# Kernel optimization log

Hardware: AMD Instinct MI355X
Metric: run time of the kernel (lower is better)

## Reference

```python
import jax, jax.numpy as jnp
import numpy as np

B, H, W, A, C = 8, 13, 13, 5, 20
ANCHORS = [[1.3221, 1.73145], [3.19275, 4.00944], [5.05587, 8.09892],
           [9.47112, 4.84053], [11.2364, 10.0071]]
L_COORD, OBJ_SCALE, NOOBJ_SCALE = 3.0, 5.0, 1.0
POS_FRAC_THRESH = 0.98


def gen_yolo_box():
    # anchor[..., 0:2] = (x_col, y_row) grid offsets, anchor[..., 2:4] = anchor (w, h)
    ys, xs = jnp.meshgrid(jnp.arange(H, dtype=jnp.float32),
                          jnp.arange(W, dtype=jnp.float32), indexing='ij')
    grid = jnp.broadcast_to(jnp.stack([xs, ys], -1)[:, :, None, :], (H, W, A, 2))
    wh = jnp.broadcast_to(jnp.asarray(ANCHORS, jnp.float32)[None, None], (H, W, A, 2))
    return jnp.concatenate([grid, wh], -1)  # [H, W, A, 4]


def decode(delta, anc, fs0, fs1):
    # delta: [..., 4] raw offsets; anc: [..., 4]; returns [x1, y1, w, h]
    w = jnp.exp(delta[..., 2]) * anc[..., 2] / fs0
    h = jnp.exp(delta[..., 3]) * anc[..., 3] / fs1
    x = (delta[..., 0] + anc[..., 0]) / fs0 - w * 0.5
    y = (delta[..., 1] + anc[..., 1]) / fs1 - h * 0.5
    return jnp.stack([x, y, w, h], -1)


def pairwise_iou(b1, b2):
    # b1: [N,4], b2: [M,4] in [x1,y1,w,h]; returns [N, M]
    b1x1, b1y1 = b1[:, 0:1], b1[:, 1:2]
    b1x2, b1y2 = b1x1 + b1[:, 2:3], b1y1 + b1[:, 3:4]
    b2x1, b2y1, b2x2, b2y2 = b2[:, 0], b2[:, 1], b2[:, 0] + b2[:, 2], b2[:, 1] + b2[:, 3]
    dx = jnp.clip(jnp.minimum(b1x2, b2x2[None, :]) - jnp.maximum(b1x1, b2x1[None, :]), 0)
    dy = jnp.clip(jnp.minimum(b1y2, b2y2[None, :]) - jnp.maximum(b1y1, b2y1[None, :]), 0)
    inter = dx * dy
    a1 = (b1x2 - b1x1) * (b1y2 - b1y1)          # [N,1]
    a2 = (b2x2 - b2x1) * (b2y2 - b2y1)          # [M]
    return inter / (a1 + a2[None, :] - inter)


def elem_iou(b1, b2):
    # elementwise IoU over [..., 4] boxes ([x1,y1,w,h])
    b1x2, b1y2 = b1[..., 0] + b1[..., 2], b1[..., 1] + b1[..., 3]
    b2x2, b2y2 = b2[..., 0] + b2[..., 2], b2[..., 1] + b2[..., 3]
    dx = jnp.clip(jnp.minimum(b1x2, b2x2) - jnp.maximum(b1[..., 0], b2[..., 0]), 0)
    dy = jnp.clip(jnp.minimum(b1y2, b2y2) - jnp.maximum(b1[..., 1], b2[..., 1]), 0)
    inter = dx * dy
    a1 = b1[..., 2] * b1[..., 3]
    a2 = b2[..., 2] * b2[..., 3]
    return inter / (a1 + a2 - inter)


def setup_inputs() -> dict:
    key = jax.random.key(0)
    ks = jax.random.split(key, 6)
    pred_cls = jax.random.normal(ks[0], (B, H, W, A, C), jnp.float32)
    pred_conf = jax.random.uniform(ks[1], (B, H, W, A, 1), jnp.float32)
    pred_bboxes = jax.random.normal(ks[2], (B, H, W, A, 4), jnp.float32)
    label_cls = jax.random.normal(ks[3], (B, H, W, A, C), jnp.float32)
    u = jax.random.uniform(ks[4], (B, H, W, A, 1), jnp.float32)
    label_conf = (u > POS_FRAC_THRESH).astype(jnp.float32)  # sparse positives
    label_bboxes = jax.random.uniform(ks[5], (B, H, W, A, 4), jnp.float32)
    return {"pred_cls": pred_cls, "pred_conf": pred_conf, "pred_bboxes": pred_bboxes,
            "label_cls": label_cls, "label_conf": label_conf, "label_bboxes": label_bboxes}


def reference(pred_cls, pred_conf, pred_bboxes, label_cls, label_conf, label_bboxes):
    dt = pred_bboxes.dtype
    fs0, fs1 = float(H), float(W)
    pos = label_conf[..., 0] > 0                 # [B,H,W,A]
    posf = pos.astype(dt)
    anc = gen_yolo_box()[None]                   # [1,H,W,A,4]

    gt_box = decode(label_bboxes, anc, fs0, fs1)   # [B,H,W,A,4]
    pred_box = decode(pred_bboxes, anc, fs0, fs1)  # [B,H,W,A,4]

    # "diagonal" IoU: each positive gt paired with the pred box at the same cell
    diag_iou = elem_iou(gt_box, pred_box)          # [B,H,W,A]
    p_conf = pred_conf[..., 0]
    loss_pos_conf = jnp.sum(posf * (p_conf - jax.lax.stop_gradient(diag_iou)) ** 2) \
        * OBJ_SCALE / B

    # dense masked pairwise IoU (gt rows masked to 0 where not positive)
    N = B * H * W * A
    iou_mat = pairwise_iou(gt_box.reshape(N, 4), pred_box.reshape(N, 4))  # [N,N]
    pos_flat = pos.reshape(N)
    iou_mat = jnp.where(pos_flat[:, None], iou_mat, jnp.zeros((), dt))
    best = jnp.max(iou_mat, axis=0)                       # per pred box
    best = jnp.where(pos_flat, jnp.ones((), dt), best)    # ious_[pos] = 1
    negf = (best < 0.6).astype(dt)
    loss_neg_conf = jnp.sum(negf * (p_conf.reshape(N) - label_conf.reshape(N)) ** 2) \
        * NOOBJ_SCALE / B

    # classification CE (sum) over positives
    logp = jax.nn.log_softmax(pred_cls, axis=-1)
    lbl = jnp.argmax(label_cls, axis=-1)
    nll = -jnp.take_along_axis(logp, lbl[..., None], axis=-1)[..., 0]
    loss_cls = jnp.sum(posf * nll) / B

    # coordinate losses over positives
    dxy = pred_bboxes[..., :2] - label_bboxes[..., :2]
    loss_x = jnp.sum(posf * dxy[..., 0] ** 2) * L_COORD / B
    loss_y = jnp.sum(posf * dxy[..., 1] ** 2) * L_COORD / B

    def huber(d):  # SmoothL1, beta=1
        ad = jnp.abs(d)
        return jnp.where(ad < 1.0, 0.5 * d * d, ad - 0.5)

    dwh = pred_bboxes[..., 2:4] - label_bboxes[..., 2:4]
    loss_w = jnp.sum(posf * huber(dwh[..., 0])) * L_COORD / B
    loss_h = jnp.sum(posf * huber(dwh[..., 1])) * L_COORD / B

    return loss_x + loss_y + loss_w + loss_h + loss_cls + loss_neg_conf + loss_pos_conf
```

## Files before the change

### kernel.cpp

```cpp
#include <hip/hip_runtime.h>

#define NB 8
#define HH 13
#define WW 13
#define AA 5
#define CC 20
#define NTOT (NB * HH * WW * AA)
#define L_COORD 3.0f
#define OBJ_SCALE 5.0f
#define INV_B (1.0f / 8.0f)
#define FS 13.0f
#define BLOCK 256
#define GRID ((NTOT + BLOCK - 1) / BLOCK)
#define CAP 4064
#define NCHUNK ((NTOT + CAP - 1) / CAP)
#define MAXITER 16

__device__ __constant__ float c_anc[AA][2] = {
    {1.3221f, 1.73145f}, {3.19275f, 4.00944f}, {5.05587f, 8.09892f},
    {9.47112f, 4.84053f}, {11.2364f, 10.0071f}};

__device__ __forceinline__ float block_reduce_sum(float v, float* sbuf) {
    for (int o = 32; o > 0; o >>= 1) v += __shfl_down(v, o);
    if ((threadIdx.x & 63) == 0) sbuf[threadIdx.x >> 6] = v;
    __syncthreads();
    float s = 0.f;
    if (threadIdx.x == 0) {
        for (int i = 0; i < (BLOCK >> 6); i++) s += sbuf[i];
    }
    return s;
}

__global__ void __launch_bounds__(BLOCK) yolo_fused_kernel(
    const float* __restrict__ pred_cls,
    const float* __restrict__ pred_conf,
    const float4* __restrict__ pred_bboxes,
    const float* __restrict__ label_cls,
    const float* __restrict__ label_conf,
    const float4* __restrict__ label_bboxes,
    float* __restrict__ out) {
    __shared__ float4 sbox[CAP];
    __shared__ int s_cnt;
    __shared__ float sred[BLOCK >> 6];

    const int tid = threadIdx.x;
    const int n   = blockIdx.x * BLOCK + tid;

    float local = 0.f;
    bool  neg   = false;
    float px1 = 0.f, py1 = 0.f, px2 = 0.f, py2 = 0.f, parea = 1.f, diffsq = 0.f;

    if (n < NTOT) {
        int a = n % AA;
        int w = (n / AA) % WW;
        int h = (n / (AA * WW)) % HH;
        float ancw = c_anc[a][0], anch = c_anc[a][1];

        float4 pb  = pred_bboxes[n];
        float  lcf = label_conf[n];
        float  pc  = pred_conf[n];

        float pw = expf(pb.z) * ancw * (1.f / FS);
        float ph = expf(pb.w) * anch * (1.f / FS);
        px1 = (pb.x + (float)w) * (1.f / FS) - pw * 0.5f;
        py1 = (pb.y + (float)h) * (1.f / FS) - ph * 0.5f;
        px2 = px1 + pw;
        py2 = py1 + ph;
        parea = pw * ph;

        if (lcf > 0.f) {
            float4 tb = label_bboxes[n];
            float gw = expf(tb.z) * ancw * (1.f / FS);
            float gh = expf(tb.w) * anch * (1.f / FS);
            float gx = (tb.x + (float)w) * (1.f / FS) - gw * 0.5f;
            float gy = (tb.y + (float)h) * (1.f / FS) - gh * 0.5f;
            float gx2 = gx + gw, gy2 = gy + gh;

            float dx = fminf(gx2, px2) - fmaxf(gx, px1); dx = fmaxf(dx, 0.f);
            float dy = fminf(gy2, py2) - fmaxf(gy, py1); dy = fmaxf(dy, 0.f);
            float inter = dx * dy;
            float iou = inter / (gw * gh + parea - inter);

            float dconf = pc - iou;
            local += OBJ_SCALE * dconf * dconf;

            const float4* lc4 = reinterpret_cast<const float4*>(label_cls) + (long)n * 5;
            const float4* pc4 = reinterpret_cast<const float4*>(pred_cls) + (long)n * 5;
            float lrow[CC], prow[CC];
            #pragma unroll
            for (int q = 0; q < 5; q++) {
                float4 v = lc4[q];
                lrow[4 * q + 0] = v.x; lrow[4 * q + 1] = v.y;
                lrow[4 * q + 2] = v.z; lrow[4 * q + 3] = v.w;
                float4 u = pc4[q];
                prow[4 * q + 0] = u.x; prow[4 * q + 1] = u.y;
                prow[4 * q + 2] = u.z; prow[4 * q + 3] = u.w;
            }
            int lbl = 0;
            float bl = lrow[0];
            #pragma unroll
            for (int i = 1; i < CC; i++) {
                if (lrow[i] > bl) { bl = lrow[i]; lbl = i; }
            }
            float mx = prow[0];
            #pragma unroll
            for (int i = 1; i < CC; i++) mx = fmaxf(mx, prow[i]);
            float s = 0.f;
            #pragma unroll
            for (int i = 0; i < CC; i++) s += expf(prow[i] - mx);
            local += mx + logf(s) - prow[lbl];

            float dxc = pb.x - tb.x, dyc = pb.y - tb.y;
            local += L_COORD * (dxc * dxc + dyc * dyc);
            float dwc = pb.z - tb.z, dhc = pb.w - tb.w;
            float adw = fabsf(dwc), adh = fabsf(dhc);
            float hw  = adw < 1.f ? 0.5f * dwc * dwc : adw - 0.5f;
            float hh2 = adh < 1.f ? 0.5f * dhc * dhc : adh - 0.5f;
            local += L_COORD * (hw + hh2);
        } else {
            neg = true;
            float d = pc - lcf;
            diffsq = d * d;
        }
    }

    float best = 0.f;
    for (int chunk = 0; chunk < NCHUNK; ++chunk) {
        const int base = chunk * CAP;
        const int rem  = min(CAP, NTOT - base);

        float cv[MAXITER];
        #pragma unroll
        for (int k = 0; k < MAXITER; k++) {
            int idx = tid + (k << 8);
            cv[k] = (idx < rem) ? label_conf[base + idx] : 0.f;
        }
        if (tid == 0) s_cnt = 0;
        __syncthreads();

        #pragma unroll
        for (int k = 0; k < MAXITER; k++) {
            int idx = tid + (k << 8);
            if (idx < rem && cv[k] > 0.f) {
                int c = base + idx;
                int a = c % AA;
                int w = (c / AA) % WW;
                int h = (c / (AA * WW)) % HH;
                float4 tb = label_bboxes[c];
                float gw = expf(tb.z) * c_anc[a][0] * (1.f / FS);
                float gh = expf(tb.w) * c_anc[a][1] * (1.f / FS);
                float gx = (tb.x + (float)w) * (1.f / FS) - gw * 0.5f;
                float gy = (tb.y + (float)h) * (1.f / FS) - gh * 0.5f;
                int s = atomicAdd(&s_cnt, 1);
                sbox[s] = make_float4(gx, gy, gx + gw, gy + gh);
            }
        }
        __syncthreads();
        const int m = s_cnt;
        if (neg) {
            #pragma unroll 4
            for (int i = 0; i < m; i++) {
                float4 g = sbox[i];
                float dx = fminf(px2, g.z) - fmaxf(px1, g.x); dx = fmaxf(dx, 0.f);
                float dy = fminf(py2, g.w) - fmaxf(py1, g.y); dy = fmaxf(dy, 0.f);
                float inter = dx * dy;
                float garea = (g.z - g.x) * (g.w - g.y);
                float iou = inter / (garea + parea - inter);
                best = fmaxf(best, iou);
            }
        }
        __syncthreads();
    }

    if (neg && best < 0.6f) local += diffsq;

    float bs = block_reduce_sum(local, sred);
    if (tid == 0) atomicAdd(out, bs * INV_B);
}

extern "C" void kernel_launch(void* const* d_in, const int* in_sizes, int n_in,
                              void* d_out, int out_size, void* d_ws, size_t ws_size,
                              hipStream_t stream) {
    const float*  pred_cls     = (const float*)d_in[0];
    const float*  pred_conf    = (const float*)d_in[1];
    const float4* pred_bboxes  = (const float4*)d_in[2];
    const float*  label_cls    = (const float*)d_in[3];
    const float*  label_conf   = (const float*)d_in[4];
    const float4* label_bboxes = (const float4*)d_in[5];
    float* out = (float*)d_out;

    yolo_fused_kernel<<<GRID, BLOCK, 0, stream>>>(
        pred_cls, pred_conf, pred_bboxes, label_cls, label_conf, label_bboxes, out);
}
```

Measured before the change: 95.72 us.

## Split into two kernels: compact positive GT boxes once, then IoU scan

```diff
diff --git a/kernel.cpp b/kernel.cpp
--- a/kernel.cpp
+++ b/kernel.cpp
@@ -12,9 +12,10 @@
 #define FS 13.0f
 #define BLOCK 256
 #define GRID ((NTOT + BLOCK - 1) / BLOCK)
-#define CAP 4064
-#define NCHUNK ((NTOT + CAP - 1) / CAP)
-#define MAXITER 16
+#define SEG BLOCK
+#define SCAP 3584
+
+#define WS_BOX_OFFSET 1024
 
 __device__ __constant__ float c_anc[AA][2] = {
     {1.3221f, 1.73145f}, {3.19275f, 4.00944f}, {5.05587f, 8.09892f},
@@ -31,45 +32,43 @@
     return s;
 }
 
-__global__ void __launch_bounds__(BLOCK) yolo_fused_kernel(
+__global__ void __launch_bounds__(BLOCK) yolo_k1(
     const float* __restrict__ pred_cls,
     const float* __restrict__ pred_conf,
     const float4* __restrict__ pred_bboxes,
     const float* __restrict__ label_cls,
     const float* __restrict__ label_conf,
     const float4* __restrict__ label_bboxes,
-    float* __restrict__ out) {
-    __shared__ float4 sbox[CAP];
-    __shared__ int s_cnt;
+    float* __restrict__ out,
+    int* __restrict__ cnt_ws,
+    float4* __restrict__ box_ws) {
+    __shared__ int s_c;
     __shared__ float sred[BLOCK >> 6];
 
     const int tid = threadIdx.x;
     const int n   = blockIdx.x * BLOCK + tid;
+    if (tid == 0) s_c = 0;
+    __syncthreads();
 
     float local = 0.f;
-    bool  neg   = false;
-    float px1 = 0.f, py1 = 0.f, px2 = 0.f, py2 = 0.f, parea = 1.f, diffsq = 0.f;
-
     if (n < NTOT) {
-        int a = n % AA;
-        int w = (n / AA) % WW;
-        int h = (n / (AA * WW)) % HH;
-        float ancw = c_anc[a][0], anch = c_anc[a][1];
-
-        float4 pb  = pred_bboxes[n];
-        float  lcf = label_conf[n];
-        float  pc  = pred_conf[n];
-
-        float pw = expf(pb.z) * ancw * (1.f / FS);
-        float ph = expf(pb.w) * anch * (1.f / FS);
-        px1 = (pb.x + (float)w) * (1.f / FS) - pw * 0.5f;
-        py1 = (pb.y + (float)h) * (1.f / FS) - ph * 0.5f;
-        px2 = px1 + pw;
-        py2 = py1 + ph;
-        parea = pw * ph;
-
+        float lcf = label_conf[n];
         if (lcf > 0.f) {
+            int a = n % AA;
+            int w = (n / AA) % WW;
+            int h = (n / (AA * WW)) % HH;
+            float ancw = c_anc[a][0], anch = c_anc[a][1];
+
+            float4 pb = pred_bboxes[n];
             float4 tb = label_bboxes[n];
+            float  pc = pred_conf[n];
+
+            float pw = expf(pb.z) * ancw * (1.f / FS);
+            float ph = expf(pb.w) * anch * (1.f / FS);
+            float px1 = (pb.x + (float)w) * (1.f / FS) - pw * 0.5f;
+            float py1 = (pb.y + (float)h) * (1.f / FS) - ph * 0.5f;
+            float px2 = px1 + pw, py2 = py1 + ph;
+
             float gw = expf(tb.z) * ancw * (1.f / FS);
             float gh = expf(tb.w) * anch * (1.f / FS);
             float gx = (tb.x + (float)w) * (1.f / FS) - gw * 0.5f;
@@ -79,8 +78,7 @@
             float dx = fminf(gx2, px2) - fmaxf(gx, px1); dx = fmaxf(dx, 0.f);
             float dy = fminf(gy2, py2) - fmaxf(gy, py1); dy = fmaxf(dy, 0.f);
             float inter = dx * dy;
-            float iou = inter / (gw * gh + parea - inter);
-
+            float iou = inter / (gw * gh + pw * ph - inter);
             float dconf = pc - iou;
             local += OBJ_SCALE * dconf * dconf;
 
@@ -99,9 +97,8 @@
             int lbl = 0;
             float bl = lrow[0];
             #pragma unroll
-            for (int i = 1; i < CC; i++) {
+            for (int i = 1; i < CC; i++)
                 if (lrow[i] > bl) { bl = lrow[i]; lbl = i; }
-            }
             float mx = prow[0];
             #pragma unroll
             for (int i = 1; i < CC; i++) mx = fmaxf(mx, prow[i]);
@@ -117,49 +114,74 @@
             float hw  = adw < 1.f ? 0.5f * dwc * dwc : adw - 0.5f;
             float hh2 = adh < 1.f ? 0.5f * dhc * dhc : adh - 0.5f;
             local += L_COORD * (hw + hh2);
-        } else {
+
+            int idx = atomicAdd(&s_c, 1);
+            box_ws[blockIdx.x * SEG + idx] = make_float4(gx, gy, gx2, gy2);
+        }
+    }
+    __syncthreads();
+    if (tid == 0) cnt_ws[blockIdx.x] = s_c;
+
+    float bs = block_reduce_sum(local, sred);
+    if (tid == 0) atomicAdd(out, bs * INV_B);
+}
+
+__global__ void __launch_bounds__(BLOCK) yolo_k2(
+    const float* __restrict__ pred_conf,
+    const float4* __restrict__ pred_bboxes,
+    const float* __restrict__ label_conf,
+    float* __restrict__ out,
+    const int* __restrict__ cnt_ws,
+    const float4* __restrict__ box_ws) {
+    __shared__ float4 sbox[SCAP];
+    __shared__ int scnt[32];
+    __shared__ float sred[BLOCK >> 6];
+
+    const int tid = threadIdx.x;
+    const int n   = blockIdx.x * BLOCK + tid;
+
+    bool  neg = false;
+    float px1 = 0.f, py1 = 0.f, px2 = 0.f, py2 = 0.f, parea = 1.f, diffsq = 0.f;
+    if (n < NTOT) {
+        float lcf = label_conf[n];
+        if (!(lcf > 0.f)) {
             neg = true;
-            float d = pc - lcf;
+            int a = n % AA;
+            int w = (n / AA) % WW;
+            int h = (n / (AA * WW)) % HH;
+            float4 pb = pred_bboxes[n];
+            float pw = expf(pb.z) * c_anc[a][0] * (1.f / FS);
+            float ph = expf(pb.w) * c_anc[a][1] * (1.f / FS);
+            px1 = (pb.x + (float)w) * (1.f / FS) - pw * 0.5f;
+            py1 = (pb.y + (float)h) * (1.f / FS) - ph * 0.5f;
+            px2 = px1 + pw;
+            py2 = py1 + ph;
+            parea = pw * ph;
+            float d = pred_conf[n] - lcf;
             diffsq = d * d;
         }
     }
 
+    if (tid < GRID) scnt[tid] = cnt_ws[tid];
+    __syncthreads();
+
+    int Mtot = 0;
+    #pragma unroll
+    for (int b = 0; b < GRID; b++) Mtot += scnt[b];
+
     float best = 0.f;
-    for (int chunk = 0; chunk < NCHUNK; ++chunk) {
-        const int base = chunk * CAP;
-        const int rem  = min(CAP, NTOT - base);
-
-        float cv[MAXITER];
+    if (Mtot <= SCAP) {
+        int off = 0;
         #pragma unroll
-        for (int k = 0; k < MAXITER; k++) {
-            int idx = tid + (k << 8);
-            cv[k] = (idx < rem) ? label_conf[base + idx] : 0.f;
-        }
-        if (tid == 0) s_cnt = 0;
+        for (int b = 0; b < GRID; b++) {
+            int cb = scnt[b];
+            if (tid < cb) sbox[off + tid] = box_ws[b * SEG + tid];
+            off += cb;
+        }
         __syncthreads();
-
-        #pragma unroll
-        for (int k = 0; k < MAXITER; k++) {
-            int idx = tid + (k << 8);
-            if (idx < rem && cv[k] > 0.f) {
-                int c = base + idx;
-                int a = c % AA;
-                int w = (c / AA) % WW;
-                int h = (c / (AA * WW)) % HH;
-                float4 tb = label_bboxes[c];
-                float gw = expf(tb.z) * c_anc[a][0] * (1.f / FS);
-                float gh = expf(tb.w) * c_anc[a][1] * (1.f / FS);
-                float gx = (tb.x + (float)w) * (1.f / FS) - gw * 0.5f;
-                float gy = (tb.y + (float)h) * (1.f / FS) - gh * 0.5f;
-                int s = atomicAdd(&s_cnt, 1);
-                sbox[s] = make_float4(gx, gy, gx + gw, gy + gh);
-            }
-        }
-        __syncthreads();
-        const int m = s_cnt;
         if (neg) {
             #pragma unroll 4
-            for (int i = 0; i < m; i++) {
+            for (int i = 0; i < Mtot; i++) {
                 float4 g = sbox[i];
                 float dx = fminf(px2, g.z) - fmaxf(px1, g.x); dx = fmaxf(dx, 0.f);
                 float dy = fminf(py2, g.w) - fmaxf(py1, g.y); dy = fmaxf(dy, 0.f);
@@ -170,11 +192,25 @@
             }
         }
         __syncthreads();
-    }
-
-    if (neg && best < 0.6f) local += diffsq;
-
-    float bs = block_reduce_sum(local, sred);
+    } else {
+        if (neg) {
+            for (int b = 0; b < GRID; b++) {
+                int cb = scnt[b];
+                for (int i = 0; i < cb; i++) {
+                    float4 g = box_ws[b * SEG + i];
+                    float dx = fminf(px2, g.z) - fmaxf(px1, g.x); dx = fmaxf(dx, 0.f);
+                    float dy = fminf(py2, g.w) - fmaxf(py1, g.y); dy = fmaxf(dy, 0.f);
+                    float inter = dx * dy;
+                    float garea = (g.z - g.x) * (g.w - g.y);
+                    float iou = inter / (garea + parea - inter);
+                    best = fmaxf(best, iou);
+                }
+            }
+        }
+    }
+
+    float contrib = (neg && best < 0.6f) ? diffsq : 0.f;
+    float bs = block_reduce_sum(contrib, sred);
     if (tid == 0) atomicAdd(out, bs * INV_B);
 }
 
@@ -189,6 +225,12 @@
     const float4* label_bboxes = (const float4*)d_in[5];
     float* out = (float*)d_out;
 
-    yolo_fused_kernel<<<GRID, BLOCK, 0, stream>>>(
-        pred_cls, pred_conf, pred_bboxes, label_cls, label_conf, label_bboxes, out);
-}
+    int*    cnt_ws = (int*)d_ws;
+    float4* box_ws = (float4*)((char*)d_ws + WS_BOX_OFFSET);
+
+    yolo_k1<<<GRID, BLOCK, 0, stream>>>(
+        pred_cls, pred_conf, pred_bboxes, label_cls, label_conf, label_bboxes,
+        out, cnt_ws, box_ws);
+    yolo_k2<<<GRID, BLOCK, 0, stream>>>(
+        pred_conf, pred_bboxes, label_conf, out, cnt_ws, box_ws);
+}
```

Measured after the change: 95.82 us. No clear change (+0.1%).

## Compact positive indices first, then tile gt boxes; replace IoU divide with threshold test

Applied to the files above, without the earlier changes.

```diff
diff --git a/kernel.cpp b/kernel.cpp
--- a/kernel.cpp
+++ b/kernel.cpp
@@ -12,9 +12,8 @@
 #define FS 13.0f
 #define BLOCK 256
 #define GRID ((NTOT + BLOCK - 1) / BLOCK)
-#define CAP 4064
-#define NCHUNK ((NTOT + CAP - 1) / CAP)
-#define MAXITER 16
+#define NSCAN 27
+#define SCAP 3072
 
 __device__ __constant__ float c_anc[AA][2] = {
     {1.3221f, 1.73145f}, {3.19275f, 4.00944f}, {5.05587f, 8.09892f},
@@ -31,7 +30,7 @@
     return s;
 }
 
-__global__ void __launch_bounds__(BLOCK) yolo_fused_kernel(
+__global__ void __launch_bounds__(BLOCK) yolo_one_kernel(
     const float* __restrict__ pred_cls,
     const float* __restrict__ pred_conf,
     const float4* __restrict__ pred_bboxes,
@@ -39,37 +38,47 @@
     const float* __restrict__ label_conf,
     const float4* __restrict__ label_bboxes,
     float* __restrict__ out) {
-    __shared__ float4 sbox[CAP];
-    __shared__ int s_cnt;
+    __shared__ unsigned short sidx[NTOT];
+    __shared__ float4 sbox[SCAP];
+    __shared__ int s_m;
     __shared__ float sred[BLOCK >> 6];
 
     const int tid = threadIdx.x;
     const int n   = blockIdx.x * BLOCK + tid;
+    const bool valid = (n < NTOT);
+    const int  nc    = valid ? n : (NTOT - 1);
+
+    float cv[NSCAN];
+    #pragma unroll
+    for (int k = 0; k < NSCAN; k++) {
+        int c = tid + (k << 8);
+        cv[k] = (c < NTOT) ? label_conf[c] : 0.f;
+    }
+    if (tid == 0) s_m = 0;
+
+    float4 pb  = pred_bboxes[nc];
+    float4 tb  = label_bboxes[nc];
+    float  lcf = label_conf[nc];
+    float  pc  = pred_conf[nc];
+
+    int a = nc % AA;
+    int w = (nc / AA) % WW;
+    int h = (nc / (AA * WW)) % HH;
+    float ancw = c_anc[a][0], anch = c_anc[a][1];
+
+    float pw = expf(pb.z) * ancw * (1.f / FS);
+    float ph = expf(pb.w) * anch * (1.f / FS);
+    float px1 = (pb.x + (float)w) * (1.f / FS) - pw * 0.5f;
+    float py1 = (pb.y + (float)h) * (1.f / FS) - ph * 0.5f;
+    float px2 = px1 + pw, py2 = py1 + ph;
+    float parea38 = 0.375f * (pw * ph);
 
     float local = 0.f;
-    bool  neg   = false;
-    float px1 = 0.f, py1 = 0.f, px2 = 0.f, py2 = 0.f, parea = 1.f, diffsq = 0.f;
+    bool  neg = false;
+    float diffsq = 0.f;
 
-    if (n < NTOT) {
-        int a = n % AA;
-        int w = (n / AA) % WW;
-        int h = (n / (AA * WW)) % HH;
-        float ancw = c_anc[a][0], anch = c_anc[a][1];
-
-        float4 pb  = pred_bboxes[n];
-        float  lcf = label_conf[n];
-        float  pc  = pred_conf[n];
-
-        float pw = expf(pb.z) * ancw * (1.f / FS);
-        float ph = expf(pb.w) * anch * (1.f / FS);
-        px1 = (pb.x + (float)w) * (1.f / FS) - pw * 0.5f;
-        py1 = (pb.y + (float)h) * (1.f / FS) - ph * 0.5f;
-        px2 = px1 + pw;
-        py2 = py1 + ph;
-        parea = pw * ph;
-
+    if (valid) {
         if (lcf > 0.f) {
-            float4 tb = label_bboxes[n];
             float gw = expf(tb.z) * ancw * (1.f / FS);
             float gh = expf(tb.w) * anch * (1.f / FS);
             float gx = (tb.x + (float)w) * (1.f / FS) - gw * 0.5f;
@@ -79,8 +88,7 @@
             float dx = fminf(gx2, px2) - fmaxf(gx, px1); dx = fmaxf(dx, 0.f);
             float dy = fminf(gy2, py2) - fmaxf(gy, py1); dy = fmaxf(dy, 0.f);
             float inter = dx * dy;
-            float iou = inter / (gw * gh + parea - inter);
-
+            float iou = inter / (gw * gh + pw * ph - inter);
             float dconf = pc - iou;
             local += OBJ_SCALE * dconf * dconf;
 
@@ -99,9 +107,8 @@
             int lbl = 0;
             float bl = lrow[0];
             #pragma unroll
-            for (int i = 1; i < CC; i++) {
+            for (int i = 1; i < CC; i++)
                 if (lrow[i] > bl) { bl = lrow[i]; lbl = i; }
-            }
             float mx = prow[0];
             #pragma unroll
             for (int i = 1; i < CC; i++) mx = fmaxf(mx, prow[i]);
@@ -124,55 +131,50 @@
         }
     }
 
-    float best = 0.f;
-    for (int chunk = 0; chunk < NCHUNK; ++chunk) {
-        const int base = chunk * CAP;
-        const int rem  = min(CAP, NTOT - base);
+    __syncthreads();
+    #pragma unroll
+    for (int k = 0; k < NSCAN; k++) {
+        int c = tid + (k << 8);
+        if (c < NTOT && cv[k] > 0.f) {
+            int p = atomicAdd(&s_m, 1);
+            sidx[p] = (unsigned short)c;
+        }
+    }
+    __syncthreads();
+    const int M = s_m;
 
-        float cv[MAXITER];
-        #pragma unroll
-        for (int k = 0; k < MAXITER; k++) {
-            int idx = tid + (k << 8);
-            cv[k] = (idx < rem) ? label_conf[base + idx] : 0.f;
-        }
-        if (tid == 0) s_cnt = 0;
-        __syncthreads();
-
-        #pragma unroll
-        for (int k = 0; k < MAXITER; k++) {
-            int idx = tid + (k << 8);
-            if (idx < rem && cv[k] > 0.f) {
-                int c = base + idx;
-                int a = c % AA;
-                int w = (c / AA) % WW;
-                int h = (c / (AA * WW)) % HH;
-                float4 tb = label_bboxes[c];
-                float gw = expf(tb.z) * c_anc[a][0] * (1.f / FS);
-                float gh = expf(tb.w) * c_anc[a][1] * (1.f / FS);
-                float gx = (tb.x + (float)w) * (1.f / FS) - gw * 0.5f;
-                float gy = (tb.y + (float)h) * (1.f / FS) - gh * 0.5f;
-                int s = atomicAdd(&s_cnt, 1);
-                sbox[s] = make_float4(gx, gy, gx + gw, gy + gh);
-            }
+    float viol = -1.f;
+    for (int base = 0; base < M; base += SCAP) {
+        const int lim = min(SCAP, M - base);
+        if (tid < lim) {
+            int j = (int)sidx[base + tid];
+            int ja = j % AA;
+            int js = j / AA;
+            int jw = js % WW;
+            int jh = (js / WW) % HH;
+            float4 gb = label_bboxes[j];
+            float gw = expf(gb.z) * c_anc[ja][0] * (1.f / FS);
+            float gh = expf(gb.w) * c_anc[ja][1] * (1.f / FS);
+            float gx = (gb.x + (float)jw) * (1.f / FS) - gw * 0.5f;
+            float gy = (gb.y + (float)jh) * (1.f / FS) - gh * 0.5f;
+            sbox[tid] = make_float4(gx, gy, gx + gw, gy + gh);
         }
         __syncthreads();
-        const int m = s_cnt;
         if (neg) {
             #pragma unroll 4
-            for (int i = 0; i < m; i++) {
+            for (int i = 0; i < lim; i++) {
                 float4 g = sbox[i];
                 float dx = fminf(px2, g.z) - fmaxf(px1, g.x); dx = fmaxf(dx, 0.f);
                 float dy = fminf(py2, g.w) - fmaxf(py1, g.y); dy = fmaxf(dy, 0.f);
                 float inter = dx * dy;
-                float garea = (g.z - g.x) * (g.w - g.y);
-                float iou = inter / (garea + parea - inter);
-                best = fmaxf(best, iou);
+                float ga38 = 0.375f * ((g.z - g.x) * (g.w - g.y));
+                viol = fmaxf(viol, inter - (ga38 + parea38));
             }
         }
         __syncthreads();
     }
 
-    if (neg && best < 0.6f) local += diffsq;
+    if (neg && viol < 0.f) local += diffsq;
 
     float bs = block_reduce_sum(local, sred);
     if (tid == 0) atomicAdd(out, bs * INV_B);
@@ -189,6 +191,6 @@
     const float4* label_bboxes = (const float4*)d_in[5];
     float* out = (float*)d_out;
 
-    yolo_fused_kernel<<<GRID, BLOCK, 0, stream>>>(
+    yolo_one_kernel<<<GRID, BLOCK, 0, stream>>>(
         pred_cls, pred_conf, pred_bboxes, label_cls, label_conf, label_bboxes, out);
 }
```

Result: faster. 84.30 us (-11.9%).
